# Kernel tuning notes

Hardware: AMD Instinct MI355X
Metric: run time of the kernel (lower is better)

## Reference

```python
import jax, jax.numpy as jnp
import numpy as np
from math import sqrt

B, S, D = 4, 2048, 1024


def setup_inputs() -> dict:
    key = jax.random.key(0)
    k1, k2, k3, k4 = jax.random.split(key, 4)
    scale = 1.0 / sqrt(D)  # roughly nn.Linear init magnitude
    x = jax.random.normal(k1, (B, S, D), dtype=jnp.float32)
    Wq = jax.random.normal(k2, (D, D), dtype=jnp.float32) * scale
    Wk = jax.random.normal(k3, (D, D), dtype=jnp.float32) * scale
    Wv = jax.random.normal(k4, (D, D), dtype=jnp.float32) * scale
    attn_mask = jnp.ones((B, S), dtype=jnp.int32)  # 1 = attend, 0 = pad
    return {"x": x, "attn_mask": attn_mask, "Wq": Wq, "Wk": Wk, "Wv": Wv}


def reference(x, attn_mask, Wq, Wk, Wv):
    # torch nn.Linear: y = x @ W.T (no bias)
    q = jnp.einsum("bsd,ed->bse", x, Wq)
    k = jnp.einsum("bsd,ed->bse", x, Wk)
    v = jnp.einsum("bsd,ed->bse", x, Wv)

    scores = jnp.einsum("bqd,bkd->bqk", q, k)  # [B, S, S]

    # causal mask (upper triangle above diagonal masked out)
    causal_mask = jnp.triu(jnp.ones((S, S), dtype=bool), k=1)  # [S, S]
    scores = jnp.where(causal_mask[None, :, :], -jnp.inf, scores)

    # padding mask: attn_mask [B, S] broadcast over query dim
    pad = (attn_mask == 0)[:, None, :]  # [B, 1, S]
    scores = jnp.where(pad, -jnp.inf, scores)

    attn_weights = jax.nn.softmax(scores / sqrt(D), axis=-1)
    return jnp.einsum("bqk,bkd->bqd", attn_weights, v)
```

## Files before the change

kernel.cpp:

```cpp
#include <hip/hip_runtime.h>
#include <stdint.h>
#include <math.h>

#define BK 64
#define LSTR 64
#define ETS 132

typedef __attribute__((ext_vector_type(8))) short short8;
typedef __attribute__((ext_vector_type(4))) float floatx4;

typedef __attribute__((address_space(3))) unsigned int lds_u32;
typedef const __attribute__((address_space(1))) unsigned int glb_u32;

__device__ __forceinline__ unsigned short f2bf(float f) {
    union { float f; unsigned u; } x; x.f = f;
    unsigned r = x.u + 0x7fffu + ((x.u >> 16) & 1u);
    return (unsigned short)(r >> 16);
}

__global__ void cvt_kernel(const float* __restrict__ x,
                           const float* __restrict__ wq,
                           const float* __restrict__ wk,
                           const float* __restrict__ wv,
                           unsigned short* __restrict__ xb,
                           unsigned short* __restrict__ wb) {
    int i4 = (blockIdx.x * 256 + threadIdx.x) * 4;
    const float* src; unsigned short* dst; int off;
    if (i4 < 8388608)       { src = x;  dst = xb;            off = i4; }
    else if (i4 < 9437184)  { src = wq; dst = wb;            off = i4 - 8388608; }
    else if (i4 < 10485760) { src = wk; dst = wb + 1048576;  off = i4 - 9437184; }
    else                    { src = wv; dst = wb + 2097152;  off = i4 - 10485760; }
    float4 v = *(const float4*)(src + off);
    ushort4 o;
    o.x = f2bf(v.x); o.y = f2bf(v.y); o.z = f2bf(v.z); o.w = f2bf(v.w);
    *(ushort4*)(dst + off) = o;
}

__device__ __forceinline__ void stage_async(unsigned short* sh, const unsigned short* g,
                                            int ld, int tid) {
#pragma unroll
    for (int it = 0; it < 4; ++it) {
        int c = it * 256 + tid;
        int row = c >> 3, cc = c & 7;
        int gcc = cc ^ (row & 7);
        __builtin_amdgcn_global_load_lds(
            (glb_u32*)(g + (size_t)row * ld + gcc * 8),
            (lds_u32*)(sh + c * 8), 16, 0, 0);
    }
}

__device__ __forceinline__ void mfma_step(const unsigned short* Ash, const unsigned short* Bsh,
                                          int lane, int wr, int wc, floatx4 acc[4][4]) {
    int lrow = lane & 15, lq = lane >> 4;
#pragma unroll
    for (int h = 0; h < 2; ++h) {
        short8 af[4], bf[4];
#pragma unroll
        for (int i = 0; i < 4; ++i) {
            int ar = wr * 64 + i * 16 + lrow;
            int br = wc * 64 + i * 16 + lrow;
            af[i] = *(const short8*)(Ash + ar * LSTR + (((h << 2) | lq) ^ (ar & 7)) * 8);
            bf[i] = *(const short8*)(Bsh + br * LSTR + (((h << 2) | lq) ^ (br & 7)) * 8);
        }
#pragma unroll
        for (int i = 0; i < 4; ++i)
#pragma unroll
            for (int j = 0; j < 4; ++j)
                acc[i][j] = __builtin_amdgcn_mfma_f32_16x16x32_bf16(af[i], bf[j], acc[i][j], 0, 0, 0);
    }
}

__global__ __launch_bounds__(256) void qkv_gemm(const unsigned short* __restrict__ Xb,
                                                const unsigned short* __restrict__ Wb,
                                                unsigned short* __restrict__ Qb,
                                                unsigned short* __restrict__ Kb,
                                                unsigned short* __restrict__ Vt) {
    __shared__ unsigned short shbuf[128 * ETS];
    unsigned short* Ash = shbuf;
    unsigned short* Bsh = shbuf + 128 * LSTR;
    int tid = threadIdx.x;
    int bm = blockIdx.x, bn = blockIdx.y;
    int lane = tid & 63, w = tid >> 6, wr = w >> 1, wc = w & 1;
    floatx4 acc[4][4];
#pragma unroll
    for (int i = 0; i < 4; ++i)
#pragma unroll
        for (int j = 0; j < 4; ++j) acc[i][j] = (floatx4){0.f, 0.f, 0.f, 0.f};

    const unsigned short* Ag = Xb + (size_t)bm * 128 * 1024;
    const unsigned short* Bg = Wb + (size_t)bn * 128 * 1024;
    for (int k0 = 0; k0 < 1024; k0 += BK) {
        __syncthreads();
        stage_async(Ash, Ag + k0, 1024, tid);
        stage_async(Bsh, Bg + k0, 1024, tid);
        __syncthreads();
        mfma_step(Ash, Bsh, lane, wr, wc, acc);
    }

    int which = bn >> 3;
    int nnb = (bn & 7) * 128;
    int lrow = lane & 15, lq = lane >> 4;
    __syncthreads();
    if (which < 2) {
#pragma unroll
        for (int i = 0; i < 4; ++i)
#pragma unroll
            for (int j = 0; j < 4; ++j)
#pragma unroll
                for (int r = 0; r < 4; ++r)
                    shbuf[(wr * 64 + i * 16 + lq * 4 + r) * ETS + wc * 64 + j * 16 + lrow] =
                        f2bf(acc[i][j][r]);
    } else {
#pragma unroll
        for (int i = 0; i < 4; ++i)
#pragma unroll
            for (int j = 0; j < 4; ++j) {
                ushort4 o;
                o.x = f2bf(acc[i][j][0]); o.y = f2bf(acc[i][j][1]);
                o.z = f2bf(acc[i][j][2]); o.w = f2bf(acc[i][j][3]);
                *(ushort4*)(shbuf + (wc * 64 + j * 16 + lrow) * ETS + wr * 64 + i * 16 + lq * 4) = o;
            }
    }
    __syncthreads();

    unsigned short* gbase; size_t gld;
    if (which == 0)      { gbase = Qb + (size_t)(bm * 128) * 1024 + nnb; gld = 1024; }
    else if (which == 1) { gbase = Kb + (size_t)(bm * 128) * 1024 + nnb; gld = 1024; }
    else { gbase = Vt + ((size_t)(bm >> 4) * 1024 + nnb) * 2048 + (bm & 15) * 128; gld = 2048; }
#pragma unroll
    for (int it = 0; it < 4; ++it) {
        int row = it * 32 + (tid >> 3), cc = tid & 7;
        uint4 v0 = *(const uint4*)(shbuf + row * ETS + cc * 8);
        uint4 v1 = *(const uint4*)(shbuf + row * ETS + 64 + cc * 8);
        *(uint4*)(gbase + (size_t)row * gld + cc * 8) = v0;
        *(uint4*)(gbase + (size_t)row * gld + 64 + cc * 8) = v1;
    }
}

__global__ __launch_bounds__(256) void scores_gemm(const unsigned short* __restrict__ Qb,
                                                   const unsigned short* __restrict__ Kb,
                                                   const int* __restrict__ mask,
                                                   float* __restrict__ Sf) {
    int u = blockIdx.x, b = blockIdx.y;
    int ti = (int)((sqrtf(8.0f * (float)u + 1.0f) - 1.0f) * 0.5f);
    while ((ti + 1) * (ti + 2) / 2 <= u) ti++;
    while (ti * (ti + 1) / 2 > u) ti--;
    int tj = u - ti * (ti + 1) / 2;

    __shared__ unsigned short shbuf[2 * 128 * LSTR];
    unsigned short* Ash = shbuf;
    unsigned short* Bsh = shbuf + 128 * LSTR;
    int tid = threadIdx.x;
    int lane = tid & 63, w = tid >> 6, wr = w >> 1, wc = w & 1;
    floatx4 acc[4][4];
#pragma unroll
    for (int i = 0; i < 4; ++i)
#pragma unroll
        for (int j = 0; j < 4; ++j) acc[i][j] = (floatx4){0.f, 0.f, 0.f, 0.f};

    const unsigned short* Ag = Qb + ((size_t)b * 2048 + ti * 128) * 1024;
    const unsigned short* Bg = Kb + ((size_t)b * 2048 + tj * 128) * 1024;
    for (int k0 = 0; k0 < 1024; k0 += BK) {
        __syncthreads();
        stage_async(Ash, Ag + k0, 1024, tid);
        stage_async(Bsh, Bg + k0, 1024, tid);
        __syncthreads();
        mfma_step(Ash, Bsh, lane, wr, wc, acc);
    }

    float* Srow = Sf + (size_t)b * 2048 * 2048;
    int lrow = lane & 15, lq = lane >> 4;
#pragma unroll
    for (int i = 0; i < 4; ++i) {
        int qrow = ti * 128 + wr * 64 + i * 16 + lq * 4;
#pragma unroll
        for (int j = 0; j < 4; ++j) {
            int n = tj * 128 + wc * 64 + j * 16 + lrow;
            int mk = mask[b * 2048 + n];
#pragma unroll
            for (int r = 0; r < 4; ++r) {
                int q = qrow + r;
                float v = acc[i][j][r] * 0.03125f;
                if (n > q || mk == 0) v = -INFINITY;
                Srow[(size_t)q * 2048 + n] = v;
            }
        }
    }
}

__global__ __launch_bounds__(256) void softmax_k(float* __restrict__ Sf) {
    int bid = blockIdx.x;
    int q = bid & 2047;
    int t = threadIdx.x;
    float* row = Sf + (size_t)bid * 2048;
    unsigned short* prow = (unsigned short*)row;
    int Lw = ((q >> 7) + 1) << 7;
    int base = t * 8;
    bool act = base < Lw;
    float v[8];
    if (act) {
        float4 a = *(const float4*)(row + base);
        float4 c = *(const float4*)(row + base + 4);
        v[0] = a.x; v[1] = a.y; v[2] = a.z; v[3] = a.w;
        v[4] = c.x; v[5] = c.y; v[6] = c.z; v[7] = c.w;
    } else {
#pragma unroll
        for (int r = 0; r < 8; ++r) v[r] = -INFINITY;
    }
    float m = -INFINITY;
#pragma unroll
    for (int r = 0; r < 8; ++r) m = fmaxf(m, v[r]);
#pragma unroll
    for (int o = 32; o >= 1; o >>= 1) m = fmaxf(m, __shfl_xor(m, o));
    __shared__ float red[4];
    if ((t & 63) == 0) red[t >> 6] = m;
    __syncthreads();
    m = fmaxf(fmaxf(red[0], red[1]), fmaxf(red[2], red[3]));

    float s = 0.f;
    if (act) {
#pragma unroll
        for (int r = 0; r < 8; ++r) { v[r] = __expf(v[r] - m); s += v[r]; }
    }
#pragma unroll
    for (int o = 32; o >= 1; o >>= 1) s += __shfl_xor(s, o);
    __syncthreads();
    if ((t & 63) == 0) red[t >> 6] = s;
    __syncthreads();
    s = red[0] + red[1] + red[2] + red[3];
    float inv = 1.f / s;
    if (act) {
        union { ushort4 u4[2]; unsigned short u[8]; } o;
#pragma unroll
        for (int r = 0; r < 8; ++r) o.u[r] = f2bf(v[r] * inv);
        *(ushort4*)(prow + base) = o.u4[0];
        *(ushort4*)(prow + base + 4) = o.u4[1];
    }
}

__global__ __launch_bounds__(256) void pv_gemm(const unsigned short* __restrict__ Pb,
                                               const unsigned short* __restrict__ Vt,
                                               float* __restrict__ out) {
    int bid = blockIdx.x;
    int half = bid >> 8, rr = bid & 255;
    int tig = rr >> 5;
    int ti = half ? tig : 15 - tig;
    int dj = (rr >> 2) & 7;
    int b  = rr & 3;
    __shared__ unsigned short shbuf[2 * 128 * LSTR];
    unsigned short* Ash = shbuf;
    unsigned short* Bsh = shbuf + 128 * LSTR;
    int tid = threadIdx.x;
    int lane = tid & 63, w = tid >> 6, wr = w >> 1, wc = w & 1;
    floatx4 acc[4][4];
#pragma unroll
    for (int i = 0; i < 4; ++i)
#pragma unroll
        for (int j = 0; j < 4; ++j) acc[i][j] = (floatx4){0.f, 0.f, 0.f, 0.f};

    const unsigned short* Ag = Pb + ((size_t)b * 2048 + ti * 128) * 4096;
    const unsigned short* Bg = Vt + ((size_t)b * 1024 + dj * 128) * 2048;
    int kend = (ti + 1) * 128;
    for (int k0 = 0; k0 < kend; k0 += BK) {
        __syncthreads();
        stage_async(Ash, Ag + k0, 4096, tid);
        stage_async(Bsh, Bg + k0, 2048, tid);
        __syncthreads();
        mfma_step(Ash, Bsh, lane, wr, wc, acc);
    }

    int lrow = lane & 15, lq = lane >> 4;
#pragma unroll
    for (int i = 0; i < 4; ++i) {
        int qrow = ti * 128 + wr * 64 + i * 16 + lq * 4;
#pragma unroll
        for (int j = 0; j < 4; ++j) {
            int d = dj * 128 + wc * 64 + j * 16 + lrow;
#pragma unroll
            for (int r = 0; r < 4; ++r)
                out[((size_t)b * 2048 + qrow + r) * 1024 + d] = acc[i][j][r];
        }
    }
}

extern "C" void kernel_launch(void* const* d_in, const int* in_sizes, int n_in,
                              void* d_out, int out_size, void* d_ws, size_t ws_size,
                              hipStream_t stream) {
    const float* x    = (const float*)d_in[0];
    const int*   mask = (const int*)d_in[1];
    const float* wq   = (const float*)d_in[2];
    const float* wk   = (const float*)d_in[3];
    const float* wv   = (const float*)d_in[4];
    float* out = (float*)d_out;
    char* ws = (char*)d_ws;

    unsigned short* Xb = (unsigned short*)(ws + 0);
    unsigned short* Wb = (unsigned short*)(ws + 16777216);
    unsigned short* Qb = (unsigned short*)(ws + 23068672);
    unsigned short* Kb = (unsigned short*)(ws + 39845888);
    unsigned short* Vt = (unsigned short*)(ws + 56623104);
    float*          Sf = (float*)(ws + 73400320);
    (void)ws_size; (void)in_sizes; (void)n_in; (void)out_size;

    cvt_kernel<<<11264, 256, 0, stream>>>(x, wq, wk, wv, Xb, Wb);
    qkv_gemm<<<dim3(64, 24), 256, 0, stream>>>(Xb, Wb, Qb, Kb, Vt);
    scores_gemm<<<dim3(136, 4), 256, 0, stream>>>(Qb, Kb, mask, Sf);
    softmax_k<<<8192, 256, 0, stream>>>(Sf);
    pv_gemm<<<512, 256, 0, stream>>>((const unsigned short*)Sf, Vt, out);
}
```

Baseline: 252.9 us.

## Fuse all stages into one cooperative persistent kernel with atomic job queues

Replaces the five separate launches (convert, QKV GEMM, scores GEMM, softmax, PV GEMM) with one cooperative kernel. Its phases are separated by grid-wide syncs, and the GEMM phases pull tiles from an atomic work counter. The aim is to remove inter-kernel launch gaps and tail effects between stages. In exchange it caps the grid at the occupancy-limited resident block count, adds grid-sync cost, and keeps job counters inside the scores workspace, which relies on that region not being overwritten.

```diff
diff --git a/kernel.cpp b/kernel.cpp
--- a/kernel.cpp
+++ b/kernel.cpp
@@ -1,6 +1,9 @@
 #include <hip/hip_runtime.h>
+#include <hip/hip_cooperative_groups.h>
 #include <stdint.h>
 #include <math.h>
+
+namespace cg = cooperative_groups;
 
 #define BK 64
 #define LSTR 64
@@ -16,24 +19,6 @@
     union { float f; unsigned u; } x; x.f = f;
     unsigned r = x.u + 0x7fffu + ((x.u >> 16) & 1u);
     return (unsigned short)(r >> 16);
-}
-
-__global__ void cvt_kernel(const float* __restrict__ x,
-                           const float* __restrict__ wq,
-                           const float* __restrict__ wk,
-                           const float* __restrict__ wv,
-                           unsigned short* __restrict__ xb,
-                           unsigned short* __restrict__ wb) {
-    int i4 = (blockIdx.x * 256 + threadIdx.x) * 4;
-    const float* src; unsigned short* dst; int off;
-    if (i4 < 8388608)       { src = x;  dst = xb;            off = i4; }
-    else if (i4 < 9437184)  { src = wq; dst = wb;            off = i4 - 8388608; }
-    else if (i4 < 10485760) { src = wk; dst = wb + 1048576;  off = i4 - 9437184; }
-    else                    { src = wv; dst = wb + 2097152;  off = i4 - 10485760; }
-    float4 v = *(const float4*)(src + off);
-    ushort4 o;
-    o.x = f2bf(v.x); o.y = f2bf(v.y); o.z = f2bf(v.z); o.w = f2bf(v.w);
-    *(ushort4*)(dst + off) = o;
 }
 
 __device__ __forceinline__ void stage_async(unsigned short* sh, const unsigned short* g,
@@ -70,16 +55,11 @@
     }
 }
 
-__global__ __launch_bounds__(256) void qkv_gemm(const unsigned short* __restrict__ Xb,
-                                                const unsigned short* __restrict__ Wb,
-                                                unsigned short* __restrict__ Qb,
-                                                unsigned short* __restrict__ Kb,
-                                                unsigned short* __restrict__ Vt) {
-    __shared__ unsigned short shbuf[128 * ETS];
+__device__ void qkv_job(int bm, int bn, const unsigned short* Xb, const unsigned short* Wb,
+                        unsigned short* Qb, unsigned short* Kb, unsigned short* Vt,
+                        unsigned short* shbuf, int tid) {
     unsigned short* Ash = shbuf;
     unsigned short* Bsh = shbuf + 128 * LSTR;
-    int tid = threadIdx.x;
-    int bm = blockIdx.x, bn = blockIdx.y;
     int lane = tid & 63, w = tid >> 6, wr = w >> 1, wc = w & 1;
     floatx4 acc[4][4];
 #pragma unroll
@@ -137,20 +117,15 @@
     }
 }
 
-__global__ __launch_bounds__(256) void scores_gemm(const unsigned short* __restrict__ Qb,
-                                                   const unsigned short* __restrict__ Kb,
-                                                   const int* __restrict__ mask,
-                                                   float* __restrict__ Sf) {
-    int u = blockIdx.x, b = blockIdx.y;
+__device__ void scores_job(int u, int b, const unsigned short* Qb, const unsigned short* Kb,
+                           const int* mask, float* Sf, unsigned short* shbuf, int tid) {
     int ti = (int)((sqrtf(8.0f * (float)u + 1.0f) - 1.0f) * 0.5f);
     while ((ti + 1) * (ti + 2) / 2 <= u) ti++;
     while (ti * (ti + 1) / 2 > u) ti--;
     int tj = u - ti * (ti + 1) / 2;
 
-    __shared__ unsigned short shbuf[2 * 128 * LSTR];
     unsigned short* Ash = shbuf;
     unsigned short* Bsh = shbuf + 128 * LSTR;
-    int tid = threadIdx.x;
     int lane = tid & 63, w = tid >> 6, wr = w >> 1, wc = w & 1;
     floatx4 acc[4][4];
 #pragma unroll
@@ -188,16 +163,16 @@
     }
 }
 
-__global__ __launch_bounds__(256) void softmax_k(float* __restrict__ Sf) {
-    int bid = blockIdx.x;
+__device__ void softmax_row(int bid, float* Sf, unsigned short* shbuf, int t) {
+    float* red = (float*)shbuf;
     int q = bid & 2047;
-    int t = threadIdx.x;
     float* row = Sf + (size_t)bid * 2048;
     unsigned short* prow = (unsigned short*)row;
     int Lw = ((q >> 7) + 1) << 7;
     int base = t * 8;
     bool act = base < Lw;
     float v[8];
+    __syncthreads();
     if (act) {
         float4 a = *(const float4*)(row + base);
         float4 c = *(const float4*)(row + base + 4);
@@ -212,7 +187,6 @@
     for (int r = 0; r < 8; ++r) m = fmaxf(m, v[r]);
 #pragma unroll
     for (int o = 32; o >= 1; o >>= 1) m = fmaxf(m, __shfl_xor(m, o));
-    __shared__ float red[4];
     if ((t & 63) == 0) red[t >> 6] = m;
     __syncthreads();
     m = fmaxf(fmaxf(red[0], red[1]), fmaxf(red[2], red[3]));
@@ -238,19 +212,11 @@
     }
 }
 
-__global__ __launch_bounds__(256) void pv_gemm(const unsigned short* __restrict__ Pb,
-                                               const unsigned short* __restrict__ Vt,
-                                               float* __restrict__ out) {
-    int bid = blockIdx.x;
-    int half = bid >> 8, rr = bid & 255;
-    int tig = rr >> 5;
-    int ti = half ? tig : 15 - tig;
-    int dj = (rr >> 2) & 7;
-    int b  = rr & 3;
-    __shared__ unsigned short shbuf[2 * 128 * LSTR];
+__device__ void pv_job(int ti, int dj, int b, const unsigned short* Pb,
+                       const unsigned short* Vt, float* out,
+                       unsigned short* shbuf, int tid) {
     unsigned short* Ash = shbuf;
     unsigned short* Bsh = shbuf + 128 * LSTR;
-    int tid = threadIdx.x;
     int lane = tid & 63, w = tid >> 6, wr = w >> 1, wc = w & 1;
     floatx4 acc[4][4];
 #pragma unroll
@@ -280,6 +246,78 @@
             for (int r = 0; r < 4; ++r)
                 out[((size_t)b * 2048 + qrow + r) * 1024 + d] = acc[i][j][r];
         }
+    }
+}
+
+__global__ __launch_bounds__(256, 4) void mega(const float* __restrict__ x,
+                                               const int* __restrict__ mask,
+                                               const float* __restrict__ wq,
+                                               const float* __restrict__ wk,
+                                               const float* __restrict__ wv,
+                                               float* __restrict__ out,
+                                               char* __restrict__ ws) {
+    __shared__ unsigned short shbuf[128 * ETS];
+    __shared__ int jobS;
+    cg::grid_group grid = cg::this_grid();
+    int blk = blockIdx.x, tid = threadIdx.x;
+    int nblk = gridDim.x;
+
+    unsigned short* Xb = (unsigned short*)(ws + 0);
+    unsigned short* Wb = (unsigned short*)(ws + 16777216);
+    unsigned short* Qb = (unsigned short*)(ws + 23068672);
+    unsigned short* Kb = (unsigned short*)(ws + 39845888);
+    unsigned short* Vt = (unsigned short*)(ws + 56623104);
+    float*          Sf = (float*)(ws + 73400320);
+    int* ctr = (int*)(Sf + 1024);
+
+    if (blk == 0 && tid < 2) ctr[tid] = nblk;
+    for (int c = blk * 256 + tid; c < 2883584; c += nblk * 256) {
+        int i4 = c * 4;
+        const float* src; unsigned short* dst; int off;
+        if (i4 < 8388608)       { src = x;  dst = Xb;            off = i4; }
+        else if (i4 < 9437184)  { src = wq; dst = Wb;            off = i4 - 8388608; }
+        else if (i4 < 10485760) { src = wk; dst = Wb + 1048576;  off = i4 - 9437184; }
+        else                    { src = wv; dst = Wb + 2097152;  off = i4 - 10485760; }
+        float4 v = *(const float4*)(src + off);
+        ushort4 o;
+        o.x = f2bf(v.x); o.y = f2bf(v.y); o.z = f2bf(v.z); o.w = f2bf(v.w);
+        *(ushort4*)(dst + off) = o;
+    }
+    grid.sync();
+
+    {
+        int job = blk;
+        while (job < 1536) {
+            qkv_job(job & 63, job >> 6, Xb, Wb, Qb, Kb, Vt, shbuf, tid);
+            if (tid == 0) jobS = atomicAdd(&ctr[0], 1);
+            __syncthreads();
+            job = jobS;
+        }
+    }
+    grid.sync();
+
+    {
+        int job = blk;
+        while (job < 544) {
+            scores_job(job % 136, job / 136, Qb, Kb, mask, Sf, shbuf, tid);
+            if (tid == 0) jobS = atomicAdd(&ctr[1], 1);
+            __syncthreads();
+            job = jobS;
+        }
+    }
+    grid.sync();
+
+    for (int row = blk; row < 8192; row += nblk)
+        softmax_row(row, Sf, shbuf, tid);
+    grid.sync();
+
+    if (blk < 512) {
+        int half = blk >> 8, rr = blk & 255;
+        int tig = rr >> 5;
+        int ti = half ? tig : 15 - tig;
+        int dj = (rr >> 2) & 7;
+        int b  = rr & 3;
+        pv_job(ti, dj, b, (const unsigned short*)Sf, Vt, out, shbuf, tid);
     }
 }
 
@@ -293,18 +331,15 @@
     const float* wv   = (const float*)d_in[4];
     float* out = (float*)d_out;
     char* ws = (char*)d_ws;
-
-    unsigned short* Xb = (unsigned short*)(ws + 0);
-    unsigned short* Wb = (unsigned short*)(ws + 16777216);
-    unsigned short* Qb = (unsigned short*)(ws + 23068672);
-    unsigned short* Kb = (unsigned short*)(ws + 39845888);
-    unsigned short* Vt = (unsigned short*)(ws + 56623104);
-    float*          Sf = (float*)(ws + 73400320);
     (void)ws_size; (void)in_sizes; (void)n_in; (void)out_size;
 
-    cvt_kernel<<<11264, 256, 0, stream>>>(x, wq, wk, wv, Xb, Wb);
-    qkv_gemm<<<dim3(64, 24), 256, 0, stream>>>(Xb, Wb, Qb, Kb, Vt);
-    scores_gemm<<<dim3(136, 4), 256, 0, stream>>>(Qb, Kb, mask, Sf);
-    softmax_k<<<8192, 256, 0, stream>>>(Sf);
-    pv_gemm<<<512, 256, 0, stream>>>((const unsigned short*)Sf, Vt, out);
-}
+    int maxPerCU = 0;
+    hipOccupancyMaxActiveBlocksPerMultiprocessor(&maxPerCU, (const void*)mega, 256, 0);
+    if (maxPerCU < 1) maxPerCU = 1;
+    if (maxPerCU > 4) maxPerCU = 4;
+    int grid = 256 * maxPerCU;
+
+    void* args[] = { (void*)&x, (void*)&mask, (void*)&wq, (void*)&wk, (void*)&wv,
+                     (void*)&out, (void*)&ws };
+    hipLaunchCooperativeKernel((void*)mega, dim3(grid), dim3(256), args, 0, stream);
+}
```

New measurement: 545.5 us. 116% more time.

## Fuse softmax exponentiation into scores GEMM and defer normalization to PV

Applied to the files above, without the earlier changes.

Removes the standalone softmax kernel. The scores GEMM epilogue now applies exp directly to the masked scaled scores with no row-max subtraction. It stages bf16 probabilities through LDS for coalesced stores and accumulates per-row sums into a global buffer via atomics. The PV GEMM divides its output by those row sums, and the probability matrix shrinks to a bf16 buffer with half the row stride. This drops the fp32 score write, the softmax read/write pass and one launch, in exchange for atomics, zero-initialising the sum buffer in the convert kernel, and possible overflow when scores are large.

```diff
diff --git a/kernel.cpp b/kernel.cpp
--- a/kernel.cpp
+++ b/kernel.cpp
@@ -23,8 +23,13 @@
                            const float* __restrict__ wk,
                            const float* __restrict__ wv,
                            unsigned short* __restrict__ xb,
-                           unsigned short* __restrict__ wb) {
+                           unsigned short* __restrict__ wb,
+                           float* __restrict__ lsum) {
     int i4 = (blockIdx.x * 256 + threadIdx.x) * 4;
+    if (blockIdx.x < 8) {
+        float4 z = (float4){0.f, 0.f, 0.f, 0.f};
+        *(float4*)(lsum + i4) = z;
+    }
     const float* src; unsigned short* dst; int off;
     if (i4 < 8388608)       { src = x;  dst = xb;            off = i4; }
     else if (i4 < 9437184)  { src = wq; dst = wb;            off = i4 - 8388608; }
@@ -140,14 +145,15 @@
 __global__ __launch_bounds__(256) void scores_gemm(const unsigned short* __restrict__ Qb,
                                                    const unsigned short* __restrict__ Kb,
                                                    const int* __restrict__ mask,
-                                                   float* __restrict__ Sf) {
+                                                   unsigned short* __restrict__ Pb,
+                                                   float* __restrict__ lsum) {
     int u = blockIdx.x, b = blockIdx.y;
     int ti = (int)((sqrtf(8.0f * (float)u + 1.0f) - 1.0f) * 0.5f);
     while ((ti + 1) * (ti + 2) / 2 <= u) ti++;
     while (ti * (ti + 1) / 2 > u) ti--;
     int tj = u - ti * (ti + 1) / 2;
 
-    __shared__ unsigned short shbuf[2 * 128 * LSTR];
+    __shared__ unsigned short shbuf[128 * ETS];
     unsigned short* Ash = shbuf;
     unsigned short* Bsh = shbuf + 128 * LSTR;
     int tid = threadIdx.x;
@@ -168,78 +174,49 @@
         mfma_step(Ash, Bsh, lane, wr, wc, acc);
     }
 
-    float* Srow = Sf + (size_t)b * 2048 * 2048;
-    int lrow = lane & 15, lq = lane >> 4;
+    int lrow = lane & 15, lq = lane >> 4;
+    int mk[4];
+#pragma unroll
+    for (int j = 0; j < 4; ++j)
+        mk[j] = mask[b * 2048 + tj * 128 + wc * 64 + j * 16 + lrow];
+
+    __syncthreads();
+    float* lrow_sum = lsum + b * 2048;
 #pragma unroll
     for (int i = 0; i < 4; ++i) {
-        int qrow = ti * 128 + wr * 64 + i * 16 + lq * 4;
-#pragma unroll
-        for (int j = 0; j < 4; ++j) {
-            int n = tj * 128 + wc * 64 + j * 16 + lrow;
-            int mk = mask[b * 2048 + n];
-#pragma unroll
-            for (int r = 0; r < 4; ++r) {
-                int q = qrow + r;
-                float v = acc[i][j][r] * 0.03125f;
-                if (n > q || mk == 0) v = -INFINITY;
-                Srow[(size_t)q * 2048 + n] = v;
+#pragma unroll
+        for (int r = 0; r < 4; ++r) {
+            int q = ti * 128 + wr * 64 + i * 16 + lq * 4 + r;
+            float rs = 0.f;
+#pragma unroll
+            for (int j = 0; j < 4; ++j) {
+                int n = tj * 128 + wc * 64 + j * 16 + lrow;
+                float p = 0.f;
+                if (n <= q && mk[j] != 0) p = __expf(acc[i][j][r] * 0.03125f);
+                rs += p;
+                shbuf[(wr * 64 + i * 16 + lq * 4 + r) * ETS + wc * 64 + j * 16 + lrow] = f2bf(p);
             }
+#pragma unroll
+            for (int o = 1; o <= 8; o <<= 1) rs += __shfl_xor(rs, o);
+            if (lrow == 0) atomicAdd(&lrow_sum[q], rs);
         }
     }
-}
-
-__global__ __launch_bounds__(256) void softmax_k(float* __restrict__ Sf) {
-    int bid = blockIdx.x;
-    int q = bid & 2047;
-    int t = threadIdx.x;
-    float* row = Sf + (size_t)bid * 2048;
-    unsigned short* prow = (unsigned short*)row;
-    int Lw = ((q >> 7) + 1) << 7;
-    int base = t * 8;
-    bool act = base < Lw;
-    float v[8];
-    if (act) {
-        float4 a = *(const float4*)(row + base);
-        float4 c = *(const float4*)(row + base + 4);
-        v[0] = a.x; v[1] = a.y; v[2] = a.z; v[3] = a.w;
-        v[4] = c.x; v[5] = c.y; v[6] = c.z; v[7] = c.w;
-    } else {
-#pragma unroll
-        for (int r = 0; r < 8; ++r) v[r] = -INFINITY;
-    }
-    float m = -INFINITY;
-#pragma unroll
-    for (int r = 0; r < 8; ++r) m = fmaxf(m, v[r]);
-#pragma unroll
-    for (int o = 32; o >= 1; o >>= 1) m = fmaxf(m, __shfl_xor(m, o));
-    __shared__ float red[4];
-    if ((t & 63) == 0) red[t >> 6] = m;
-    __syncthreads();
-    m = fmaxf(fmaxf(red[0], red[1]), fmaxf(red[2], red[3]));
-
-    float s = 0.f;
-    if (act) {
-#pragma unroll
-        for (int r = 0; r < 8; ++r) { v[r] = __expf(v[r] - m); s += v[r]; }
-    }
-#pragma unroll
-    for (int o = 32; o >= 1; o >>= 1) s += __shfl_xor(s, o);
-    __syncthreads();
-    if ((t & 63) == 0) red[t >> 6] = s;
-    __syncthreads();
-    s = red[0] + red[1] + red[2] + red[3];
-    float inv = 1.f / s;
-    if (act) {
-        union { ushort4 u4[2]; unsigned short u[8]; } o;
-#pragma unroll
-        for (int r = 0; r < 8; ++r) o.u[r] = f2bf(v[r] * inv);
-        *(ushort4*)(prow + base) = o.u4[0];
-        *(ushort4*)(prow + base + 4) = o.u4[1];
+    __syncthreads();
+
+    unsigned short* gbase = Pb + ((size_t)b * 2048 + ti * 128) * 2048 + tj * 128;
+#pragma unroll
+    for (int it = 0; it < 4; ++it) {
+        int row = it * 32 + (tid >> 3), cc = tid & 7;
+        uint4 v0 = *(const uint4*)(shbuf + row * ETS + cc * 8);
+        uint4 v1 = *(const uint4*)(shbuf + row * ETS + 64 + cc * 8);
+        *(uint4*)(gbase + (size_t)row * 2048 + cc * 8) = v0;
+        *(uint4*)(gbase + (size_t)row * 2048 + 64 + cc * 8) = v1;
     }
 }
 
 __global__ __launch_bounds__(256) void pv_gemm(const unsigned short* __restrict__ Pb,
                                                const unsigned short* __restrict__ Vt,
+                                               const float* __restrict__ lsum,
                                                float* __restrict__ out) {
     int bid = blockIdx.x;
     int half = bid >> 8, rr = bid & 255;
@@ -258,12 +235,12 @@
 #pragma unroll
         for (int j = 0; j < 4; ++j) acc[i][j] = (floatx4){0.f, 0.f, 0.f, 0.f};
 
-    const unsigned short* Ag = Pb + ((size_t)b * 2048 + ti * 128) * 4096;
+    const unsigned short* Ag = Pb + ((size_t)b * 2048 + ti * 128) * 2048;
     const unsigned short* Bg = Vt + ((size_t)b * 1024 + dj * 128) * 2048;
     int kend = (ti + 1) * 128;
     for (int k0 = 0; k0 < kend; k0 += BK) {
         __syncthreads();
-        stage_async(Ash, Ag + k0, 4096, tid);
+        stage_async(Ash, Ag + k0, 2048, tid);
         stage_async(Bsh, Bg + k0, 2048, tid);
         __syncthreads();
         mfma_step(Ash, Bsh, lane, wr, wc, acc);
@@ -274,11 +251,13 @@
     for (int i = 0; i < 4; ++i) {
         int qrow = ti * 128 + wr * 64 + i * 16 + lq * 4;
 #pragma unroll
-        for (int j = 0; j < 4; ++j) {
-            int d = dj * 128 + wc * 64 + j * 16 + lrow;
-#pragma unroll
-            for (int r = 0; r < 4; ++r)
-                out[((size_t)b * 2048 + qrow + r) * 1024 + d] = acc[i][j][r];
+        for (int r = 0; r < 4; ++r) {
+            float invl = 1.f / lsum[b * 2048 + qrow + r];
+#pragma unroll
+            for (int j = 0; j < 4; ++j) {
+                int d = dj * 128 + wc * 64 + j * 16 + lrow;
+                out[((size_t)b * 2048 + qrow + r) * 1024 + d] = acc[i][j][r] * invl;
+            }
         }
     }
 }
@@ -299,12 +278,12 @@
     unsigned short* Qb = (unsigned short*)(ws + 23068672);
     unsigned short* Kb = (unsigned short*)(ws + 39845888);
     unsigned short* Vt = (unsigned short*)(ws + 56623104);
-    float*          Sf = (float*)(ws + 73400320);
+    unsigned short* Pb = (unsigned short*)(ws + 73400320);
+    float*        lsum = (float*)(ws + 106954752);
     (void)ws_size; (void)in_sizes; (void)n_in; (void)out_size;
 
-    cvt_kernel<<<11264, 256, 0, stream>>>(x, wq, wk, wv, Xb, Wb);
+    cvt_kernel<<<11264, 256, 0, stream>>>(x, wq, wk, wv, Xb, Wb, lsum);
     qkv_gemm<<<dim3(64, 24), 256, 0, stream>>>(Xb, Wb, Qb, Kb, Vt);
-    scores_gemm<<<dim3(136, 4), 256, 0, stream>>>(Qb, Kb, mask, Sf);
-    softmax_k<<<8192, 256, 0, stream>>>(Sf);
-    pv_gemm<<<512, 256, 0, stream>>>((const unsigned short*)Sf, Vt, out);
-}
+    scores_gemm<<<dim3(136, 4), 256, 0, stream>>>(Qb, Kb, mask, Pb, lsum);
+    pv_gemm<<<512, 256, 0, stream>>>(Pb, Vt, lsum, out);
+}
```

New measurement: 247.3 us. -2.2%, faster.
